# Kernel optimization log

Measured on AMD Instinct MI355X. Metric: run time of the kernel, lower is better.

The kernel has to match this reference:

```python
import jax, jax.numpy as jnp
import numpy as np

KNN_K = 16
EPS = 1e-5


def _knn_idx(p, k):
    # p: [B,3,N] -> idx [B,N,k] of nearest neighbors (self excluded)
    pt = jnp.swapaxes(p, 1, 2)                      # [B,N,3]
    xx = jnp.sum(pt * pt, axis=-1)                  # [B,N]
    inner = jnp.einsum('bnd,bmd->bnm', pt, pt)      # [B,N,N]
    dist = -(xx[:, :, None] - 2.0 * inner + xx[:, None, :])  # -||pi-pj||^2
    N = pt.shape[1]
    dist = dist - 1e9 * jnp.eye(N, dtype=dist.dtype)
    return jax.lax.top_k(dist, k)[1]


def _ln(x, g, b):
    mu = jnp.mean(x, axis=-1, keepdims=True)
    var = jnp.mean((x - mu) ** 2, axis=-1, keepdims=True)
    return (x - mu) * jax.lax.rsqrt(var + EPS) * g + b


_gather = jax.vmap(lambda a, i: a[i])  # a:[N,C], i:[N,k] -> [N,k,C]


def setup_inputs() -> dict:
    key = jax.random.key(0)
    ks = jax.random.split(key, 24)
    Cin, C, B, N = 64, 128, 8, 2048
    s = lambda k_, shp, fan: jax.random.normal(k_, shp, jnp.float32) * (1.0 / np.sqrt(fan))
    return {
        'x': jax.random.normal(ks[0], (B, Cin, N), jnp.float32),
        'p': jax.random.normal(ks[1], (B, 3, N), jnp.float32),
        'Win': s(ks[2], (C, Cin), Cin), 'bin_': jnp.zeros((C,), jnp.float32),
        'Wq': s(ks[3], (C, C), C), 'Wk': s(ks[4], (C, C), C), 'Wv': s(ks[5], (C, C), C),
        'Wd1': s(ks[6], (C, 3), 3), 'bd1': jnp.zeros((C,), jnp.float32),
        'Wd2': s(ks[7], (C, C), C), 'bd2': jnp.zeros((C,), jnp.float32),
        'Wa': s(ks[8], (C, C), C), 'ba': jnp.zeros((C,), jnp.float32),
        'g1': jnp.ones((C,), jnp.float32), 'b1': jnp.zeros((C,), jnp.float32),
        'g2': jnp.ones((C,), jnp.float32), 'b2': jnp.zeros((C,), jnp.float32),
        'Wf1': s(ks[9], (4 * C, C), C), 'bf1': jnp.zeros((4 * C,), jnp.float32),
        'Wf2': s(ks[10], (C, 4 * C), 4 * C), 'bf2': jnp.zeros((C,), jnp.float32),
    }


def reference(x, p, Win, bin_, Wq, Wk, Wv, Wd1, bd1, Wd2, bd2, Wa, ba,
              g1, b1, g2, b2, Wf1, bf1, Wf2, bf2) -> jnp.ndarray:
    B, _, N = x.shape
    k = min(KNN_K, max(1, N - 1))
    # in_proj (conv1x1 == per-point linear); work in [B,N,C]
    h = jnp.einsum('oc,bcn->bno', Win, x) + bin_          # [B,N,C]
    hn = _ln(h, g1, b1)
    idx = _knn_idx(p, k)                                  # [B,N,k] (int)
    q = hn @ Wq.T                                         # [B,N,C]
    k_all = hn @ Wk.T
    v_all = hn @ Wv.T
    k_j = _gather(k_all, idx)                             # [B,N,k,C]
    v_j = _gather(v_all, idx)
    pt = jnp.swapaxes(p, 1, 2)                            # [B,N,3]
    p_j = _gather(pt, idx)                                # [B,N,k,3]
    rel = pt[:, :, None, :] - p_j                         # [B,N,k,3]
    d = jax.nn.relu(rel @ Wd1.T + bd1) @ Wd2.T + bd2      # [B,N,k,C]
    logits = (q[:, :, None, :] - k_j + d) @ Wa.T + ba     # [B,N,k,C]
    a = jax.nn.softmax(logits, axis=2)                    # softmax over neighbors
    y = jnp.sum(a * (v_j + d), axis=2)                    # [B,N,C]
    h = h + y
    h2 = _ln(h, g2, b2)
    h = h + jax.nn.relu(h2 @ Wf1.T + bf1) @ Wf2.T + bf2
    return jnp.swapaxes(h, 1, 2)                          # [B,C,N]
```

## Files before the change

### kernel.cpp

```cpp
#include <hip/hip_runtime.h>

typedef __bf16 bf16_t;
typedef __bf16 bf16x8 __attribute__((ext_vector_type(8)));
typedef __bf16 bf16x2 __attribute__((ext_vector_type(2)));
typedef float  f32x4  __attribute__((ext_vector_type(4)));

#define MFMA16(a,b,c) __builtin_amdgcn_mfma_f32_16x16x32_bf16((a),(b),(c),0,0,0)

#define BB 8
#define NN 2048
#define CC 128
#define CIN 64
#define KNB 16
#define BNT (BB*NN)

static __device__ __forceinline__ int remap256(int x) { return ((x & 7) << 5) | (x >> 3); }

static __device__ __forceinline__ bf16x8 cvt8(const float* src) {
  f32x4 a0 = *(const f32x4*)src;
  f32x4 a1 = *(const f32x4*)(src + 4);
  bf16x8 fr;
  fr[0] = (__bf16)a0[0]; fr[1] = (__bf16)a0[1]; fr[2] = (__bf16)a0[2]; fr[3] = (__bf16)a0[3];
  fr[4] = (__bf16)a1[0]; fr[5] = (__bf16)a1[1]; fr[6] = (__bf16)a1[2]; fr[7] = (__bf16)a1[3];
  return fr;
}

__global__ __launch_bounds__(256) void inproj_compw_k(
    const float* __restrict__ x, const float* __restrict__ Win, const float* __restrict__ bin,
    const float* __restrict__ g1, const float* __restrict__ b1,
    bf16_t* __restrict__ hb, bf16_t* __restrict__ hnb,
    const float* __restrict__ Wq, const float* __restrict__ Wk, const float* __restrict__ Wv,
    const float* __restrict__ Wd2, const float* __restrict__ Wa,
    const float* __restrict__ Wf1, const float* __restrict__ Wf2,
    bf16_t* __restrict__ Wqb, bf16_t* __restrict__ Wkb, bf16_t* __restrict__ Wvb,
    bf16_t* __restrict__ Wd2b, bf16_t* __restrict__ Wab,
    bf16_t* __restrict__ Wf1b, bf16_t* __restrict__ Wf2b) {
  __shared__ bf16_t As[64 * 72];
  __shared__ bf16_t Bs[128 * 72];
  __shared__ float hs[64 * 132];
  int t = threadIdx.x;
  if (blockIdx.x >= 256) {
    int bi = blockIdx.x - 256;
    int mat = bi >> 3, xi = bi & 7;
    int nel = (mat >= 5) ? 65536 : 16384;
    const float* S = mat == 0 ? Wq : mat == 1 ? Wk : mat == 2 ? Wv : mat == 3 ? Wd2
                   : mat == 4 ? Wa : mat == 5 ? Wf1 : Wf2;
    bf16_t* D = mat == 0 ? Wqb : mat == 1 ? Wkb : mat == 2 ? Wvb : mat == 3 ? Wd2b
              : mat == 4 ? Wab : mat == 5 ? Wf1b : Wf2b;
    for (int i = xi * 256 + t; i * 8 < nel; i += 2048)
      *(bf16x8*)(D + i * 8) = cvt8(S + i * 8);
    return;
  }
  int lane = t & 63, w = t >> 6, quad = lane >> 4, l15 = lane & 15;
  int mBase = remap256(blockIdx.x) * 64;
  int b = mBase >> 11, n0 = mBase & (NN - 1);
  const float* xb = x + (size_t)b * CIN * NN;
  {
    int k = t >> 2, part = t & 3;
    #pragma unroll
    for (int i = 0; i < 4; ++i) {
      f32x4 v = *(const f32x4*)(xb + (size_t)k * NN + n0 + part * 16 + i * 4);
      #pragma unroll
      for (int j2 = 0; j2 < 4; ++j2) As[(part * 16 + i * 4 + j2) * 72 + k] = (__bf16)v[j2];
    }
  }
  {
    int row = t >> 1, seg = (t & 1) * 32;
    #pragma unroll
    for (int i = 0; i < 4; ++i)
      *(bf16x8*)(&Bs[row * 72 + seg + i * 8]) = cvt8(Win + (size_t)row * CIN + seg + i * 8);
  }
  __syncthreads();
  f32x4 acc[2][4] = {};
  #pragma unroll
  for (int s = 0; s < 2; ++s) {
    bf16x8 af[4];
    #pragma unroll
    for (int mt = 0; mt < 4; ++mt)
      af[mt] = *(const bf16x8*)(&As[(mt * 16 + l15) * 72 + s * 32 + quad * 8]);
    #pragma unroll
    for (int t2 = 0; t2 < 2; ++t2) {
      bf16x8 bfr = *(const bf16x8*)(&Bs[((w * 2 + t2) * 16 + l15) * 72 + s * 32 + quad * 8]);
      #pragma unroll
      for (int mt = 0; mt < 4; ++mt) acc[t2][mt] = MFMA16(af[mt], bfr, acc[t2][mt]);
    }
  }
  #pragma unroll
  for (int t2 = 0; t2 < 2; ++t2) {
    int col = (w * 2 + t2) * 16 + l15;
    float bv = bin[col];
    #pragma unroll
    for (int mt = 0; mt < 4; ++mt)
      #pragma unroll
      for (int reg = 0; reg < 4; ++reg)
        hs[(mt * 16 + quad * 4 + reg) * 132 + col] = acc[t2][mt][reg] + bv;
  }
  __syncthreads();
  {
    int row = t >> 2, c0 = (t & 3) * 32;
    float v[32];
    #pragma unroll
    for (int i = 0; i < 8; ++i) *(f32x4*)(v + i * 4) = *(const f32x4*)(&hs[row * 132 + c0 + i * 4]);
    float s1 = 0.f, s2 = 0.f;
    #pragma unroll
    for (int i = 0; i < 32; ++i) { s1 += v[i]; s2 += v[i] * v[i]; }
    s1 += __shfl_xor(s1, 1); s1 += __shfl_xor(s1, 2);
    s2 += __shfl_xor(s2, 1); s2 += __shfl_xor(s2, 2);
    float mu = s1 * (1.f / CC);
    float var = s2 * (1.f / CC) - mu * mu;
    float rs = rsqrtf(var + 1e-5f);
    bf16_t* hrow = hb + (size_t)(mBase + row) * CC + c0;
    #pragma unroll
    for (int i = 0; i < 4; ++i) {
      bf16x8 ho;
      #pragma unroll
      for (int j = 0; j < 8; ++j) ho[j] = (__bf16)v[i * 8 + j];
      *(bf16x8*)(hrow + i * 8) = ho;
    }
    bf16_t* hnrow = hnb + (size_t)(mBase + row) * CC + c0;
    #pragma unroll
    for (int i = 0; i < 4; ++i) {
      f32x4 g4a = ((const f32x4*)g1)[(c0 >> 2) + i * 2],     g4b = ((const f32x4*)g1)[(c0 >> 2) + i * 2 + 1];
      f32x4 b4a = ((const f32x4*)b1)[(c0 >> 2) + i * 2],     b4b = ((const f32x4*)b1)[(c0 >> 2) + i * 2 + 1];
      bf16x8 o;
      #pragma unroll
      for (int j = 0; j < 4; ++j) o[j]     = (__bf16)((v[i * 8 + j]     - mu) * rs * g4a[j] + b4a[j]);
      #pragma unroll
      for (int j = 0; j < 4; ++j) o[4 + j] = (__bf16)((v[i * 8 + 4 + j] - mu) * rs * g4b[j] + b4b[j]);
      *(bf16x8*)(hnrow + i * 8) = o;
    }
  }
}

static __device__ __forceinline__ void cas(double& a, double& b) {
  double lo = fmin(a, b), hi = fmax(a, b); a = lo; b = hi;
}
#define S8(K,o) \
  cas(K[o+0],K[o+1]); cas(K[o+2],K[o+3]); cas(K[o+4],K[o+5]); cas(K[o+6],K[o+7]); \
  cas(K[o+0],K[o+2]); cas(K[o+1],K[o+3]); cas(K[o+4],K[o+6]); cas(K[o+5],K[o+7]); \
  cas(K[o+1],K[o+2]); cas(K[o+5],K[o+6]); \
  cas(K[o+0],K[o+4]); cas(K[o+1],K[o+5]); cas(K[o+2],K[o+6]); cas(K[o+3],K[o+7]); \
  cas(K[o+2],K[o+4]); cas(K[o+3],K[o+5]); \
  cas(K[o+1],K[o+2]); cas(K[o+3],K[o+4]); cas(K[o+5],K[o+6]);
#define M8(K,a,b) \
  K[a+0]=fmin(K[a+0],K[b+7]); K[a+1]=fmin(K[a+1],K[b+6]); K[a+2]=fmin(K[a+2],K[b+5]); K[a+3]=fmin(K[a+3],K[b+4]); \
  K[a+4]=fmin(K[a+4],K[b+3]); K[a+5]=fmin(K[a+5],K[b+2]); K[a+6]=fmin(K[a+6],K[b+1]); K[a+7]=fmin(K[a+7],K[b+0]); \
  cas(K[a+0],K[a+4]); cas(K[a+1],K[a+5]); cas(K[a+2],K[a+6]); cas(K[a+3],K[a+7]); \
  cas(K[a+0],K[a+2]); cas(K[a+1],K[a+3]); cas(K[a+4],K[a+6]); cas(K[a+5],K[a+7]); \
  cas(K[a+0],K[a+1]); cas(K[a+2],K[a+3]); cas(K[a+4],K[a+5]); cas(K[a+6],K[a+7]);

static __device__ void knn_impl(float* sp, const float* __restrict__ p,
                                int* __restrict__ idxo, int bid) {
  float* px = sp; float* py = sp + NN; float* pz = sp + 2 * NN;
  int t = threadIdx.x;
  int b = bid >> 9;
  int g = bid & 511;
  const float* pb = p + (size_t)b * 3 * NN;
  for (int i = t; i < NN; i += 256) { px[i] = pb[i]; py[i] = pb[NN + i]; pz[i] = pb[2 * NN + i]; }
  __syncthreads();
  int w = t >> 6, lane = t & 63;
  int n = g * 4 + w;
  float pnx = px[n], pny = py[n], pnz = pz[n];
  double key[32];
  #pragma unroll
  for (int s = 0; s < 32; ++s) {
    int m = s * 64 + lane;
    float dx = pnx - px[m], dy = pny - py[m], dz = pnz - pz[m];
    float dist = dx * dx + dy * dy + dz * dz;
    unsigned db = (m == n) ? 0x7F800000u : __float_as_uint(dist);
    key[s] = __hiloint2double((int)db, m);
  }
  S8(key, 0); S8(key, 8); S8(key, 16); S8(key, 24);
  M8(key, 0, 8); M8(key, 16, 24); M8(key, 0, 16);
  const double DINF = __hiloint2double(0x7F900000, 0);
  int* myout = idxo + ((size_t)b * NN + n) * KNB;
  #pragma unroll 1
  for (int r = 0; r < 16; ++r) {
    double gm = key[0];
    #pragma unroll
    for (int off = 1; off < 64; off <<= 1) {
      double o = __shfl_xor(gm, off);
      gm = fmin(gm, o);
    }
    if (lane == 0) myout[r] = __double2loint(gm);
    bool win = (key[0] == gm);
    key[0] = win ? key[1] : key[0];
    key[1] = win ? key[2] : key[1];
    key[2] = win ? key[3] : key[2];
    key[3] = win ? key[4] : key[3];
    key[4] = win ? key[5] : key[4];
    key[5] = win ? key[6] : key[5];
    key[6] = win ? key[7] : key[6];
    key[7] = win ? DINF   : key[7];
  }
}

template<int EPI>
static __device__ void gemm_body(bf16_t* As, bf16_t* Bs,
    const bf16_t* __restrict__ Ab, const bf16_t* __restrict__ Wb, const float* __restrict__ bias,
    float* __restrict__ outF, bf16_t* __restrict__ outB, const bf16_t* __restrict__ resid,
    int mBase, int nBase, int Ncol, int Kdim) {
  int t = threadIdx.x;
  int lane = t & 63, w = t >> 6, quad = lane >> 4, l15 = lane & 15;
  int r = t >> 2, seg = (t & 3) * 8;
  f32x4 acc[4] = {{0,0,0,0},{0,0,0,0},{0,0,0,0},{0,0,0,0}};
  for (int k0 = 0; k0 < Kdim; k0 += 32) {
    __syncthreads();
    *(bf16x8*)(&As[r * 40 + seg]) = *(const bf16x8*)(Ab + (size_t)(mBase + r) * Kdim + k0 + seg);
    *(bf16x8*)(&Bs[r * 40 + seg]) = *(const bf16x8*)(Wb + (size_t)(nBase + r) * Kdim + k0 + seg);
    __syncthreads();
    bf16x8 bfr = *(const bf16x8*)(&Bs[(w * 16 + l15) * 40 + quad * 8]);
    #pragma unroll
    for (int mt = 0; mt < 4; ++mt) {
      bf16x8 afr = *(const bf16x8*)(&As[(mt * 16 + l15) * 40 + quad * 8]);
      acc[mt] = MFMA16(afr, bfr, acc[mt]);
    }
  }
  int n = nBase + w * 16 + l15;
  float bv = bias ? bias[n] : 0.f;
  #pragma unroll
  for (int mt = 0; mt < 4; ++mt) {
    #pragma unroll
    for (int reg = 0; reg < 4; ++reg) {
      int m = mBase + mt * 16 + quad * 4 + reg;
      float val = acc[mt][reg] + bv;
      if (EPI == 1) {
        outB[(size_t)m * Ncol + n] = (__bf16)fmaxf(val, 0.f);
      } else if (EPI == 3) {
        outB[(size_t)m * Ncol + n] = (__bf16)val;
      } else {
        val += (float)resid[(size_t)m * CC + n];
        int bo = m >> 11, np = m & (NN - 1);
        outF[((size_t)bo * CC + n) * NN + np] = val;
      }
    }
  }
}

template<int EPI>
__global__ __launch_bounds__(256) void gemm_k(
    const bf16_t* __restrict__ Ab, const bf16_t* __restrict__ Wb, const float* __restrict__ bias,
    float* __restrict__ outF, bf16_t* __restrict__ outB, const bf16_t* __restrict__ resid,
    int Ncol, int Kdim) {
  __shared__ bf16_t As[64 * 40];
  __shared__ bf16_t Bs[64 * 40];
  gemm_body<EPI>(As, Bs, Ab, Wb, bias, outF, outB, resid,
                 remap256(blockIdx.x) * 64, blockIdx.y * 64, Ncol, Kdim);
}

__global__ __launch_bounds__(256) void knn_qkv_k(
    const float* __restrict__ p, int* __restrict__ idxo,
    const bf16_t* __restrict__ hnb,
    const bf16_t* __restrict__ Wqb, const bf16_t* __restrict__ Wkb, const bf16_t* __restrict__ Wvb,
    bf16_t* __restrict__ qb, bf16_t* __restrict__ kb, bf16_t* __restrict__ vb) {
  __shared__ __align__(16) char smem[3 * NN * 4];
  if (blockIdx.x < 4096) {
    knn_impl((float*)smem, p, idxo, blockIdx.x);
  } else {
    bf16_t* As = (bf16_t*)smem;
    bf16_t* Bs = As + 64 * 40;
    int bx = blockIdx.x - 4096;
    int yy = bx >> 8, xx = bx & 255;
    int sel = yy >> 1;
    int mB = remap256(xx) * 64, nB = (yy & 1) * 64;
    if (sel == 0)      gemm_body<3>(As, Bs, hnb, Wqb, nullptr, nullptr, qb, nullptr, mB, nB, CC, CC);
    else if (sel == 1) gemm_body<3>(As, Bs, hnb, Wkb, nullptr, nullptr, kb, nullptr, mB, nB, CC, CC);
    else               gemm_body<3>(As, Bs, hnb, Wvb, nullptr, nullptr, vb, nullptr, mB, nB, CC, CC);
  }
}

__global__ __launch_bounds__(256, 4) void attn_k(
    const bf16_t* __restrict__ qbuf, const bf16_t* __restrict__ kbuf, const bf16_t* __restrict__ vbuf,
    const float* __restrict__ p, const int* __restrict__ idx,
    const float* __restrict__ Wd1, const float* __restrict__ bd1,
    const bf16_t* __restrict__ Wd2b, const float* __restrict__ bd2,
    const bf16_t* __restrict__ Wab, const float* __restrict__ ba,
    const float* __restrict__ g2, const float* __restrict__ b2,
    const bf16_t* __restrict__ hb, bf16_t* __restrict__ hresb, bf16_t* __restrict__ h2) {
  __shared__ bf16_t ts[64 * 136];
  __shared__ float hrs[4 * 128];
  __shared__ f32x4 wd1s[128];
  __shared__ f32x4 rels4[64];
  __shared__ int idxs[64];
  int t = threadIdx.x;
  int lane = t & 63, w = t >> 6, quad = lane >> 4, l15 = lane & 15;
  int batch = blockIdx.x & 7, grp = blockIdx.x >> 3;
  int bn0 = batch * NN + grp * 4;
  int b = batch;
  const float* pb = p + (size_t)b * 3 * NN;
  int col0 = w * 32 + l15;
  int col1 = col0 + 16;

  bf16x8 Bd[2][4];
  #pragma unroll
  for (int t2 = 0; t2 < 2; ++t2) {
    int row = w * 32 + t2 * 16 + l15;
    #pragma unroll
    for (int s = 0; s < 4; ++s)
      Bd[t2][s] = *(const bf16x8*)(Wd2b + (size_t)row * CC + s * 32 + quad * 8);
  }

  if (t < 64) {
    int jj = idx[(size_t)bn0 * KNB + t];
    idxs[t] = jj;
    int npt = grp * 4 + (t >> 4);
    f32x4 rv;
    rv[0] = pb[npt]          - pb[jj];
    rv[1] = pb[NN + npt]     - pb[NN + jj];
    rv[2] = pb[2 * NN + npt] - pb[2 * NN + jj];
    rv[3] = 0.f;
    rels4[t] = rv;
  }
  if (t < 128) {
    f32x4 wv;
    wv[0] = Wd1[t * 3]; wv[1] = Wd1[t * 3 + 1]; wv[2] = Wd1[t * 3 + 2]; wv[3] = bd1[t];
    wd1s[t] = wv;
  }
  __syncthreads();

  float qv[2][4];
  #pragma unroll
  for (int mt = 0; mt < 4; ++mt) {
    qv[0][mt] = (float)qbuf[(size_t)(bn0 + mt) * CC + col0];
    qv[1][mt] = (float)qbuf[(size_t)(bn0 + mt) * CC + col1];
  }
  float kreg[2][4][4];
  #pragma unroll
  for (int mt = 0; mt < 4; ++mt)
    #pragma unroll
    for (int reg = 0; reg < 4; ++reg) {
      size_t base = (size_t)(b * NN + idxs[mt * 16 + quad * 4 + reg]) * CC;
      kreg[0][mt][reg] = (float)kbuf[base + col0];
      kreg[1][mt][reg] = (float)kbuf[base + col1];
    }

  f32x4 relv[4];
  #pragma unroll
  for (int mt = 0; mt < 4; ++mt) relv[mt] = rels4[mt * 16 + l15];
  f32x4 accd[2][4] = {};
  #pragma unroll
  for (int s = 0; s < 4; ++s) {
    bf16x8 af[4];
    #pragma unroll
    for (int j = 0; j < 8; ++j) {
      f32x4 wv = wd1s[s * 32 + quad * 8 + j];
      #pragma unroll
      for (int mt = 0; mt < 4; ++mt) {
        float tv = fmaf(wv[0], relv[mt][0], fmaf(wv[1], relv[mt][1], fmaf(wv[2], relv[mt][2], wv[3])));
        af[mt][j] = (__bf16)fmaxf(tv, 0.f);
      }
    }
    #pragma unroll
    for (int t2 = 0; t2 < 2; ++t2)
      #pragma unroll
      for (int mt = 0; mt < 4; ++mt)
        accd[t2][mt] = MFMA16(af[mt], Bd[t2][s], accd[t2][mt]);
  }

  {
    float b2v0 = bd2[col0], b2v1 = bd2[col1];
    #pragma unroll
    for (int mt = 0; mt < 4; ++mt)
      #pragma unroll
      for (int reg = 0; reg < 4; ++reg) {
        int row = mt * 16 + quad * 4 + reg;
        float d0 = accd[0][mt][reg] + b2v0;
        float d1 = accd[1][mt][reg] + b2v1;
        accd[0][mt][reg] = d0;
        accd[1][mt][reg] = d1;
        ts[row * 136 + col0] = (__bf16)(qv[0][mt] - kreg[0][mt][reg] + d0);
        ts[row * 136 + col1] = (__bf16)(qv[1][mt] - kreg[1][mt][reg] + d1);
      }
  }
  __syncthreads();

  float vreg[2][4][4];
  #pragma unroll
  for (int mt = 0; mt < 4; ++mt)
    #pragma unroll
    for (int reg = 0; reg < 4; ++reg) {
      size_t base = (size_t)(b * NN + idxs[mt * 16 + quad * 4 + reg]) * CC;
      vreg[0][mt][reg] = (float)vbuf[base + col0];
      vreg[1][mt][reg] = (float)vbuf[base + col1];
    }
  float hv[2][4];
  if (quad == 0) {
    #pragma unroll
    for (int mt = 0; mt < 4; ++mt) {
      hv[0][mt] = (float)hb[(size_t)(bn0 + mt) * CC + col0];
      hv[1][mt] = (float)hb[(size_t)(bn0 + mt) * CC + col1];
    }
  }
  bf16x8 Ba[2][4];
  #pragma unroll
  for (int t2 = 0; t2 < 2; ++t2) {
    int row = w * 32 + t2 * 16 + l15;
    #pragma unroll
    for (int s = 0; s < 4; ++s)
      Ba[t2][s] = *(const bf16x8*)(Wab + (size_t)row * CC + s * 32 + quad * 8);
  }

  f32x4 accl[2][4] = {};
  #pragma unroll
  for (int s = 0; s < 4; ++s) {
    bf16x8 af[4];
    #pragma unroll
    for (int mt = 0; mt < 4; ++mt)
      af[mt] = *(const bf16x8*)(&ts[(mt * 16 + l15) * 136 + s * 32 + quad * 8]);
    #pragma unroll
    for (int t2 = 0; t2 < 2; ++t2)
      #pragma unroll
      for (int mt = 0; mt < 4; ++mt)
        accl[t2][mt] = MFMA16(af[mt], Ba[t2][s], accl[t2][mt]);
  }

  #pragma unroll
  for (int t2 = 0; t2 < 2; ++t2) {
    int col = t2 ? col1 : col0;
    float bav = ba[col];
    #pragma unroll
    for (int mt = 0; mt < 4; ++mt) {
      float lv0 = accl[t2][mt][0] + bav, lv1 = accl[t2][mt][1] + bav;
      float lv2 = accl[t2][mt][2] + bav, lv3 = accl[t2][mt][3] + bav;
      float mx = fmaxf(fmaxf(lv0, lv1), fmaxf(lv2, lv3));
      mx = fmaxf(mx, __shfl_xor(mx, 16));
      mx = fmaxf(mx, __shfl_xor(mx, 32));
      float e0 = __expf(lv0 - mx), e1 = __expf(lv1 - mx);
      float e2 = __expf(lv2 - mx), e3 = __expf(lv3 - mx);
      float ss = e0 + e1 + e2 + e3;
      ss += __shfl_xor(ss, 16); ss += __shfl_xor(ss, 32);
      float yv = e0 * (vreg[t2][mt][0] + accd[t2][mt][0])
               + e1 * (vreg[t2][mt][1] + accd[t2][mt][1])
               + e2 * (vreg[t2][mt][2] + accd[t2][mt][2])
               + e3 * (vreg[t2][mt][3] + accd[t2][mt][3]);
      yv += __shfl_xor(yv, 16); yv += __shfl_xor(yv, 32);
      if (quad == 0) {
        float hvv = hv[t2][mt] + yv / ss;
        hresb[(size_t)(bn0 + mt) * CC + col] = (__bf16)hvv;
        hrs[mt * 128 + col] = hvv;
      }
    }
  }
  __syncthreads();

  {
    int c0 = lane * 2;
    float v0 = hrs[w * 128 + c0], v1 = hrs[w * 128 + c0 + 1];
    float s1 = v0 + v1, s2 = v0 * v0 + v1 * v1;
    #pragma unroll
    for (int off = 1; off < 64; off <<= 1) { s1 += __shfl_xor(s1, off); s2 += __shfl_xor(s2, off); }
    float mu = s1 * (1.f / CC);
    float var = s2 * (1.f / CC) - mu * mu;
    float rs = rsqrtf(var + 1e-5f);
    bf16x2 o;
    o[0] = (__bf16)((v0 - mu) * rs * g2[c0] + b2[c0]);
    o[1] = (__bf16)((v1 - mu) * rs * g2[c0 + 1] + b2[c0 + 1]);
    *(bf16x2*)(h2 + (size_t)(bn0 + w) * CC + c0) = o;
  }
}

extern "C" void kernel_launch(void* const* d_in, const int* in_sizes, int n_in,
                              void* d_out, int out_size, void* d_ws, size_t ws_size,
                              hipStream_t stream) {
  const float* x   = (const float*)d_in[0];
  const float* p   = (const float*)d_in[1];
  const float* Win = (const float*)d_in[2];
  const float* bin = (const float*)d_in[3];
  const float* Wq  = (const float*)d_in[4];
  const float* Wk  = (const float*)d_in[5];
  const float* Wv  = (const float*)d_in[6];
  const float* Wd1 = (const float*)d_in[7];
  const float* bd1 = (const float*)d_in[8];
  const float* Wd2 = (const float*)d_in[9];
  const float* bd2 = (const float*)d_in[10];
  const float* Wa  = (const float*)d_in[11];
  const float* ba  = (const float*)d_in[12];
  const float* g1  = (const float*)d_in[13];
  const float* b1  = (const float*)d_in[14];
  const float* g2  = (const float*)d_in[15];
  const float* b2  = (const float*)d_in[16];
  const float* Wf1 = (const float*)d_in[17];
  const float* bf1 = (const float*)d_in[18];
  const float* Wf2 = (const float*)d_in[19];
  const float* bf2 = (const float*)d_in[20];
  float* out = (float*)d_out;

  const size_t SZ = (size_t)BNT * CC;
  float* wsf = (float*)d_ws;
  bf16_t* hb    = (bf16_t*)wsf;
  bf16_t* hnb   = (bf16_t*)(wsf + SZ / 2);
  bf16_t* hresb = hnb;
  bf16_t* qb    = (bf16_t*)(wsf + SZ);
  bf16_t* kb    = (bf16_t*)(wsf + SZ + SZ / 2);
  bf16_t* vb    = (bf16_t*)(wsf + 2 * SZ);
  bf16_t* g     = (bf16_t*)(wsf + SZ);
  bf16_t* h2    = (bf16_t*)(wsf + 3 * SZ);
  int*    idxw  = (int*)(wsf + 3 * SZ + SZ / 2);
  bf16_t* Wqb   = (bf16_t*)(idxw + (size_t)BNT * KNB);
  bf16_t* Wkb   = Wqb  + 16384;
  bf16_t* Wvb   = Wkb  + 16384;
  bf16_t* Wd2b  = Wvb  + 16384;
  bf16_t* Wab   = Wd2b + 16384;
  bf16_t* Wf1b  = Wab  + 16384;
  bf16_t* Wf2b  = Wf1b + 65536;

  inproj_compw_k<<<256 + 56, 256, 0, stream>>>(x, Win, bin, g1, b1, hb, hnb,
                                               Wq, Wk, Wv, Wd2, Wa, Wf1, Wf2,
                                               Wqb, Wkb, Wvb, Wd2b, Wab, Wf1b, Wf2b);
  knn_qkv_k<<<4096 + 1536, 256, 0, stream>>>(p, idxw, hnb, Wqb, Wkb, Wvb, qb, kb, vb);
  attn_k<<<BNT / 4, 256, 0, stream>>>(qb, kb, vb, p, idxw, Wd1, bd1, Wd2b, bd2, Wab, ba,
                                      g2, b2, hb, hresb, h2);
  gemm_k<1><<<dim3(BNT / 64, 8), 256, 0, stream>>>(h2, Wf1b, bf1, nullptr, g, nullptr, 4 * CC, CC);
  gemm_k<2><<<dim3(BNT / 64, 2), 256, 0, stream>>>(g, Wf2b, bf2, out, nullptr, hresb, CC, 4 * CC);
}
```

Baseline: 308.2 us.

## Widen GEMM tiles to reuse A fragments across Q/K/V and FFN outputs

Replaces the generic 64x64 GEMM with specialized kernels where each block loads its A tile once and computes several 64-wide output groups: QKV fused into one block per column half, FFN1 computing 256 columns per block, FFN2 computing all 128 columns. This cuts redundant A-tile global loads and block count. It also lowers attn_k launch bounds from 4 to 3 waves per SIMD. The cost is more accumulator registers and fewer blocks, which can reduce occupancy and parallelism.

```diff
diff --git a/kernel.cpp b/kernel.cpp
--- a/kernel.cpp
+++ b/kernel.cpp
@@ -195,59 +195,6 @@
   }
 }
 
-template<int EPI>
-static __device__ void gemm_body(bf16_t* As, bf16_t* Bs,
-    const bf16_t* __restrict__ Ab, const bf16_t* __restrict__ Wb, const float* __restrict__ bias,
-    float* __restrict__ outF, bf16_t* __restrict__ outB, const bf16_t* __restrict__ resid,
-    int mBase, int nBase, int Ncol, int Kdim) {
-  int t = threadIdx.x;
-  int lane = t & 63, w = t >> 6, quad = lane >> 4, l15 = lane & 15;
-  int r = t >> 2, seg = (t & 3) * 8;
-  f32x4 acc[4] = {{0,0,0,0},{0,0,0,0},{0,0,0,0},{0,0,0,0}};
-  for (int k0 = 0; k0 < Kdim; k0 += 32) {
-    __syncthreads();
-    *(bf16x8*)(&As[r * 40 + seg]) = *(const bf16x8*)(Ab + (size_t)(mBase + r) * Kdim + k0 + seg);
-    *(bf16x8*)(&Bs[r * 40 + seg]) = *(const bf16x8*)(Wb + (size_t)(nBase + r) * Kdim + k0 + seg);
-    __syncthreads();
-    bf16x8 bfr = *(const bf16x8*)(&Bs[(w * 16 + l15) * 40 + quad * 8]);
-    #pragma unroll
-    for (int mt = 0; mt < 4; ++mt) {
-      bf16x8 afr = *(const bf16x8*)(&As[(mt * 16 + l15) * 40 + quad * 8]);
-      acc[mt] = MFMA16(afr, bfr, acc[mt]);
-    }
-  }
-  int n = nBase + w * 16 + l15;
-  float bv = bias ? bias[n] : 0.f;
-  #pragma unroll
-  for (int mt = 0; mt < 4; ++mt) {
-    #pragma unroll
-    for (int reg = 0; reg < 4; ++reg) {
-      int m = mBase + mt * 16 + quad * 4 + reg;
-      float val = acc[mt][reg] + bv;
-      if (EPI == 1) {
-        outB[(size_t)m * Ncol + n] = (__bf16)fmaxf(val, 0.f);
-      } else if (EPI == 3) {
-        outB[(size_t)m * Ncol + n] = (__bf16)val;
-      } else {
-        val += (float)resid[(size_t)m * CC + n];
-        int bo = m >> 11, np = m & (NN - 1);
-        outF[((size_t)bo * CC + n) * NN + np] = val;
-      }
-    }
-  }
-}
-
-template<int EPI>
-__global__ __launch_bounds__(256) void gemm_k(
-    const bf16_t* __restrict__ Ab, const bf16_t* __restrict__ Wb, const float* __restrict__ bias,
-    float* __restrict__ outF, bf16_t* __restrict__ outB, const bf16_t* __restrict__ resid,
-    int Ncol, int Kdim) {
-  __shared__ bf16_t As[64 * 40];
-  __shared__ bf16_t Bs[64 * 40];
-  gemm_body<EPI>(As, Bs, Ab, Wb, bias, outF, outB, resid,
-                 remap256(blockIdx.x) * 64, blockIdx.y * 64, Ncol, Kdim);
-}
-
 __global__ __launch_bounds__(256) void knn_qkv_k(
     const float* __restrict__ p, int* __restrict__ idxo,
     const bf16_t* __restrict__ hnb,
@@ -256,20 +203,147 @@
   __shared__ __align__(16) char smem[3 * NN * 4];
   if (blockIdx.x < 4096) {
     knn_impl((float*)smem, p, idxo, blockIdx.x);
-  } else {
-    bf16_t* As = (bf16_t*)smem;
-    bf16_t* Bs = As + 64 * 40;
-    int bx = blockIdx.x - 4096;
-    int yy = bx >> 8, xx = bx & 255;
-    int sel = yy >> 1;
-    int mB = remap256(xx) * 64, nB = (yy & 1) * 64;
-    if (sel == 0)      gemm_body<3>(As, Bs, hnb, Wqb, nullptr, nullptr, qb, nullptr, mB, nB, CC, CC);
-    else if (sel == 1) gemm_body<3>(As, Bs, hnb, Wkb, nullptr, nullptr, kb, nullptr, mB, nB, CC, CC);
-    else               gemm_body<3>(As, Bs, hnb, Wvb, nullptr, nullptr, vb, nullptr, mB, nB, CC, CC);
-  }
-}
-
-__global__ __launch_bounds__(256, 4) void attn_k(
+    return;
+  }
+  bf16_t* As = (bf16_t*)smem;
+  bf16_t* Bs0 = As + 2560;
+  bf16_t* Bs1 = Bs0 + 2560;
+  bf16_t* Bs2 = Bs1 + 2560;
+  int t = threadIdx.x;
+  int lane = t & 63, w = t >> 6, quad = lane >> 4, l15 = lane & 15;
+  int bx = blockIdx.x - 4096;
+  int xx = bx & 255, yy = bx >> 8;
+  int mB = remap256(xx) * 64, nB = yy * 64;
+  int r = t >> 2, seg = (t & 3) * 8;
+  f32x4 acc[3][4] = {};
+  for (int k0 = 0; k0 < CC; k0 += 32) {
+    __syncthreads();
+    *(bf16x8*)(&As[r * 40 + seg])  = *(const bf16x8*)(hnb + (size_t)(mB + r) * CC + k0 + seg);
+    *(bf16x8*)(&Bs0[r * 40 + seg]) = *(const bf16x8*)(Wqb + (size_t)(nB + r) * CC + k0 + seg);
+    *(bf16x8*)(&Bs1[r * 40 + seg]) = *(const bf16x8*)(Wkb + (size_t)(nB + r) * CC + k0 + seg);
+    *(bf16x8*)(&Bs2[r * 40 + seg]) = *(const bf16x8*)(Wvb + (size_t)(nB + r) * CC + k0 + seg);
+    __syncthreads();
+    bf16x8 af[4];
+    #pragma unroll
+    for (int mt = 0; mt < 4; ++mt)
+      af[mt] = *(const bf16x8*)(&As[(mt * 16 + l15) * 40 + quad * 8]);
+    bf16x8 b0 = *(const bf16x8*)(&Bs0[(w * 16 + l15) * 40 + quad * 8]);
+    bf16x8 b1 = *(const bf16x8*)(&Bs1[(w * 16 + l15) * 40 + quad * 8]);
+    bf16x8 b2 = *(const bf16x8*)(&Bs2[(w * 16 + l15) * 40 + quad * 8]);
+    #pragma unroll
+    for (int mt = 0; mt < 4; ++mt) {
+      acc[0][mt] = MFMA16(af[mt], b0, acc[0][mt]);
+      acc[1][mt] = MFMA16(af[mt], b1, acc[1][mt]);
+      acc[2][mt] = MFMA16(af[mt], b2, acc[2][mt]);
+    }
+  }
+  int n = nB + w * 16 + l15;
+  #pragma unroll
+  for (int mat = 0; mat < 3; ++mat) {
+    bf16_t* dst = mat == 0 ? qb : mat == 1 ? kb : vb;
+    #pragma unroll
+    for (int mt = 0; mt < 4; ++mt)
+      #pragma unroll
+      for (int reg = 0; reg < 4; ++reg) {
+        int m = mB + mt * 16 + quad * 4 + reg;
+        dst[(size_t)m * CC + n] = (__bf16)acc[mat][mt][reg];
+      }
+  }
+}
+
+__global__ __launch_bounds__(256) void ffn1_k(
+    const bf16_t* __restrict__ h2, const bf16_t* __restrict__ Wf1b,
+    const float* __restrict__ bf1, bf16_t* __restrict__ g) {
+  __shared__ bf16_t As[64 * 40];
+  __shared__ bf16_t Bs[4][64 * 40];
+  int t = threadIdx.x;
+  int lane = t & 63, w = t >> 6, quad = lane >> 4, l15 = lane & 15;
+  int mB = remap256(blockIdx.x) * 64;
+  int nG = blockIdx.y * 256;
+  int r = t >> 2, seg = (t & 3) * 8;
+  f32x4 acc[4][4] = {};
+  for (int k0 = 0; k0 < CC; k0 += 32) {
+    __syncthreads();
+    *(bf16x8*)(&As[r * 40 + seg]) = *(const bf16x8*)(h2 + (size_t)(mB + r) * CC + k0 + seg);
+    #pragma unroll
+    for (int gi = 0; gi < 4; ++gi)
+      *(bf16x8*)(&Bs[gi][r * 40 + seg]) =
+          *(const bf16x8*)(Wf1b + (size_t)(nG + gi * 64 + r) * CC + k0 + seg);
+    __syncthreads();
+    bf16x8 af[4];
+    #pragma unroll
+    for (int mt = 0; mt < 4; ++mt)
+      af[mt] = *(const bf16x8*)(&As[(mt * 16 + l15) * 40 + quad * 8]);
+    #pragma unroll
+    for (int gi = 0; gi < 4; ++gi) {
+      bf16x8 bfr = *(const bf16x8*)(&Bs[gi][(w * 16 + l15) * 40 + quad * 8]);
+      #pragma unroll
+      for (int mt = 0; mt < 4; ++mt)
+        acc[gi][mt] = MFMA16(af[mt], bfr, acc[gi][mt]);
+    }
+  }
+  #pragma unroll
+  for (int gi = 0; gi < 4; ++gi) {
+    int n = nG + gi * 64 + w * 16 + l15;
+    float bv = bf1[n];
+    #pragma unroll
+    for (int mt = 0; mt < 4; ++mt)
+      #pragma unroll
+      for (int reg = 0; reg < 4; ++reg) {
+        int m = mB + mt * 16 + quad * 4 + reg;
+        g[(size_t)m * (4 * CC) + n] = (__bf16)fmaxf(acc[gi][mt][reg] + bv, 0.f);
+      }
+  }
+}
+
+__global__ __launch_bounds__(256) void ffn2_k(
+    const bf16_t* __restrict__ g, const bf16_t* __restrict__ Wf2b,
+    const float* __restrict__ bf2, const bf16_t* __restrict__ resid,
+    float* __restrict__ out) {
+  __shared__ bf16_t As[64 * 40];
+  __shared__ bf16_t Bs[2][64 * 40];
+  int t = threadIdx.x;
+  int lane = t & 63, w = t >> 6, quad = lane >> 4, l15 = lane & 15;
+  int mB = remap256(blockIdx.x) * 64;
+  int r = t >> 2, seg = (t & 3) * 8;
+  f32x4 acc[2][4] = {};
+  for (int k0 = 0; k0 < 4 * CC; k0 += 32) {
+    __syncthreads();
+    *(bf16x8*)(&As[r * 40 + seg]) = *(const bf16x8*)(g + (size_t)(mB + r) * (4 * CC) + k0 + seg);
+    #pragma unroll
+    for (int hh = 0; hh < 2; ++hh)
+      *(bf16x8*)(&Bs[hh][r * 40 + seg]) =
+          *(const bf16x8*)(Wf2b + (size_t)(hh * 64 + r) * (4 * CC) + k0 + seg);
+    __syncthreads();
+    bf16x8 af[4];
+    #pragma unroll
+    for (int mt = 0; mt < 4; ++mt)
+      af[mt] = *(const bf16x8*)(&As[(mt * 16 + l15) * 40 + quad * 8]);
+    #pragma unroll
+    for (int hh = 0; hh < 2; ++hh) {
+      bf16x8 bfr = *(const bf16x8*)(&Bs[hh][(w * 16 + l15) * 40 + quad * 8]);
+      #pragma unroll
+      for (int mt = 0; mt < 4; ++mt)
+        acc[hh][mt] = MFMA16(af[mt], bfr, acc[hh][mt]);
+    }
+  }
+  #pragma unroll
+  for (int hh = 0; hh < 2; ++hh) {
+    int n = hh * 64 + w * 16 + l15;
+    float bv = bf2[n];
+    #pragma unroll
+    for (int mt = 0; mt < 4; ++mt)
+      #pragma unroll
+      for (int reg = 0; reg < 4; ++reg) {
+        int m = mB + mt * 16 + quad * 4 + reg;
+        float val = acc[hh][mt][reg] + bv + (float)resid[(size_t)m * CC + n];
+        int bo = m >> 11, np = m & (NN - 1);
+        out[((size_t)bo * CC + n) * NN + np] = val;
+      }
+  }
+}
+
+__global__ __launch_bounds__(256, 3) void attn_k(
     const bf16_t* __restrict__ qbuf, const bf16_t* __restrict__ kbuf, const bf16_t* __restrict__ vbuf,
     const float* __restrict__ p, const int* __restrict__ idx,
     const float* __restrict__ Wd1, const float* __restrict__ bd1,
@@ -507,9 +581,9 @@
   inproj_compw_k<<<256 + 56, 256, 0, stream>>>(x, Win, bin, g1, b1, hb, hnb,
                                                Wq, Wk, Wv, Wd2, Wa, Wf1, Wf2,
                                                Wqb, Wkb, Wvb, Wd2b, Wab, Wf1b, Wf2b);
-  knn_qkv_k<<<4096 + 1536, 256, 0, stream>>>(p, idxw, hnb, Wqb, Wkb, Wvb, qb, kb, vb);
+  knn_qkv_k<<<4096 + 512, 256, 0, stream>>>(p, idxw, hnb, Wqb, Wkb, Wvb, qb, kb, vb);
   attn_k<<<BNT / 4, 256, 0, stream>>>(qb, kb, vb, p, idxw, Wd1, bd1, Wd2b, bd2, Wab, ba,
                                       g2, b2, hb, hresb, h2);
-  gemm_k<1><<<dim3(BNT / 64, 8), 256, 0, stream>>>(h2, Wf1b, bf1, nullptr, g, nullptr, 4 * CC, CC);
-  gemm_k<2><<<dim3(BNT / 64, 2), 256, 0, stream>>>(g, Wf2b, bf2, out, nullptr, hresb, CC, 4 * CC);
-}
+  ffn1_k<<<dim3(256, 2), 256, 0, stream>>>(h2, Wf1b, bf1, g);
+  ffn2_k<<<256, 256, 0, stream>>>(g, Wf2b, bf2, hresb, out);
+}
```

Measured after the change: 268.9 us. 1.15x faster.
